# Optimization experiments

Hardware: AMD Instinct MI355X
Metric: run time of the kernel (lower is better)

Reference implementation:

```python
import jax, jax.numpy as jnp
import numpy as np

B, DIM, H, W, HEAD = 8, 512, 32, 32, 8
DH = DIM // HEAD
N = H * W


def setup_inputs() -> dict:
    key = jax.random.key(0)
    ks = jax.random.split(key, 9)
    s = 0.05  # keep conv-weight scale modest so softmax logits are sane
    return {
        "x": jax.random.normal(ks[0], (B, DIM, H, W), jnp.float32),
        "wq_w": jax.random.normal(ks[1], (DIM, DIM), jnp.float32) * s,
        "wq_b": jax.random.normal(ks[2], (DIM,), jnp.float32) * s,
        "wk_w": jax.random.normal(ks[3], (DIM, DIM), jnp.float32) * s,
        "wk_b": jax.random.normal(ks[4], (DIM,), jnp.float32) * s,
        "wv_w": jax.random.normal(ks[5], (DIM, DIM), jnp.float32) * s,
        "wv_b": jax.random.normal(ks[6], (DIM,), jnp.float32) * s,
        "r_h": jax.random.normal(ks[7], (1, HEAD, DH, 1, H), jnp.float32),
        "r_w": jax.random.normal(ks[8], (1, HEAD, DH, W, 1), jnp.float32),
    }


def reference(x, wq_w, wq_b, wk_w, wk_b, wv_w, wv_b, r_h, r_w):
    b, dim, h, w = x.shape
    head = r_h.shape[1]
    dh = dim // head
    n = h * w

    def conv1x1(inp, wgt, bias):
        # 1x1 conv == channel-mixing matmul
        return jnp.einsum('bchw,oc->bohw', inp, wgt) + bias[None, :, None, None]

    q = conv1x1(x, wq_w, wq_b).reshape(b, head, dh, n).transpose(0, 1, 3, 2)  # [b,h,n,d]
    k = conv1x1(x, wk_w, wk_b).reshape(b, head, dh, n)                        # [b,h,d,n]
    v = conv1x1(x, wv_w, wv_b).reshape(b, head, dh, n)                        # [b,h,d,n]

    # relative position term: (1,head,dh,1,H)+(1,head,dh,W,1) -> (1,head,dh,W*H)
    r = (r_h + r_w).reshape(head, dh, n)

    content_position = jnp.einsum('bhnd,hdm->bhnm', q, r)
    content_content = jnp.einsum('bhnd,bhdm->bhnm', q, k)
    # faithful odd reduction: softmax over the whole flattened (head*n*n) per batch row
    energy = (content_content + content_position).reshape(b, -1)
    attention = jax.nn.softmax(energy, axis=-1).reshape(b, head, n, n)

    feature = jnp.einsum('bhdn,bhnm->bhdm', v, attention).reshape(b, dim, h, w)
    # AvgPool2d(kernel=2, stride=2)
    out = feature.reshape(b, dim, h // 2, 2, w // 2, 2).mean(axis=(3, 5))
    return out
```

## Files before the change

### kernel.cpp

```cpp
#include <hip/hip_runtime.h>
#include <hip/hip_bf16.h>
#include <math.h>

#define BB   8
#define DIMC 512
#define HEAD 8
#define DH   64
#define NN   1024
#define HW   32

typedef __attribute__((ext_vector_type(8))) __bf16 bf16x8;
typedef __attribute__((ext_vector_type(4))) float  f32x4;

#define MFMA16(a, b, c) __builtin_amdgcn_mfma_f32_16x16x32_bf16((a), (b), (c), 0, 0, 0)

__device__ __forceinline__ int SW(int row, int col) {
    return (row << 6) + (col ^ ((row & 7) << 3));
}

__device__ __forceinline__ unsigned short bfh(float v) {
    unsigned int u = __float_as_uint(v);
    return (unsigned short)((u + 0x7fffu + ((u >> 16) & 1u)) >> 16);
}
__device__ __forceinline__ float bf2f(unsigned short h) {
    return __uint_as_float(((unsigned int)h) << 16);
}

__global__ __launch_bounds__(256)
void prep_x(const float* __restrict__ x,
            unsigned short* __restrict__ XTh, unsigned short* __restrict__ XTl)
{
    const int tid = threadIdx.x;
    const int nt = blockIdx.x;
    const int ct = blockIdx.y;
    const int b  = blockIdx.z;
    const int c0 = ct << 6, n0 = nt << 6;

    __shared__ float XsT[64][68];

    #pragma unroll
    for (int p = 0; p < 4; ++p) {
        int idx = tid + (p << 8);
        int cr = idx >> 4;
        int nc4 = (idx & 15) << 2;
        float4 v = *(const float4*)&x[((size_t)b * DIMC + c0 + cr) * NN + n0 + nc4];
        XsT[nc4 + 0][cr] = v.x;
        XsT[nc4 + 1][cr] = v.y;
        XsT[nc4 + 2][cr] = v.z;
        XsT[nc4 + 3][cr] = v.w;
    }
    __syncthreads();
    #pragma unroll
    for (int p = 0; p < 4; ++p) {
        int idx = tid + (p << 8);
        int n = idx >> 4;
        int c4 = (idx & 15) << 2;
        float4 v = *(const float4*)&XsT[n][c4];
        float vv[4] = {v.x, v.y, v.z, v.w};
        union { unsigned short u[4]; uint2 w; } ph, pl;
        #pragma unroll
        for (int j = 0; j < 4; ++j) {
            unsigned short hh = bfh(vv[j]);
            ph.u[j] = hh;
            pl.u[j] = bfh(vv[j] - bf2f(hh));
        }
        size_t off = ((size_t)(b * NN + n0 + n)) * DIMC + c0 + c4;
        *(uint2*)&XTh[off] = ph.w;
        *(uint2*)&XTl[off] = pl.w;
    }
}

__global__ __launch_bounds__(256)
void prep_w(const float* __restrict__ wq, const float* __restrict__ wk,
            const float* __restrict__ wv,
            unsigned short* __restrict__ Wh, unsigned short* __restrict__ Wl)
{
    const int z = blockIdx.y;
    const float* src = (z == 0) ? wq : (z == 1) ? wk : wv;
    const size_t zb = (size_t)z * DIMC * DIMC;
    #pragma unroll
    for (int p = 0; p < 4; ++p) {
        size_t i = (size_t)blockIdx.x * 4096 + (p << 10) + (threadIdx.x << 2);
        float4 v = *(const float4*)&src[i];
        float vv[4] = {v.x, v.y, v.z, v.w};
        union { unsigned short u[4]; uint2 w; } ph, pl;
        #pragma unroll
        for (int j = 0; j < 4; ++j) {
            unsigned short hh = bfh(vv[j]);
            ph.u[j] = hh;
            pl.u[j] = bfh(vv[j] - bf2f(hh));
        }
        *(uint2*)&Wh[zb + i] = ph.w;
        *(uint2*)&Wl[zb + i] = pl.w;
    }
}

__global__ __launch_bounds__(256)
void qkv_gemm(const unsigned short* __restrict__ XTh, const unsigned short* __restrict__ XTl,
              const unsigned short* __restrict__ Wh, const unsigned short* __restrict__ Wl,
              const float* __restrict__ wq_b, const float* __restrict__ wk_b,
              const float* __restrict__ wv_b,
              const float* __restrict__ r_h, const float* __restrict__ r_w,
              unsigned short* __restrict__ Qh, unsigned short* __restrict__ Ql,
              unsigned short* __restrict__ Kh, unsigned short* __restrict__ Kl,
              unsigned short* __restrict__ Vh, unsigned short* __restrict__ Vl)
{
    const int tid = threadIdx.x;
    const int z = blockIdx.z, hd = blockIdx.y;
    const int gn = blockIdx.x << 7;
    const int b = gn >> 10, posb = gn & 1023;
    const int oB = hd << 6;
    const int lane = tid & 63, w = tid >> 6;

    __shared__ __align__(16) unsigned short sm[24576];
    unsigned short* Ah = sm;
    unsigned short* Al = sm + 4096;
    unsigned short* Bh = sm + 8192;
    unsigned short* Bl = sm + 16384;

    const float* bias = (z == 0) ? wq_b : (z == 1) ? wk_b : wv_b;
    const unsigned short* wsh = Wh + (size_t)z * DIMC * DIMC + (size_t)oB * DIMC;
    const unsigned short* wsl = Wl + (size_t)z * DIMC * DIMC + (size_t)oB * DIMC;
    const unsigned short* xth = XTh + ((size_t)(b * NN + posb)) * DIMC;
    const unsigned short* xtl = XTl + ((size_t)(b * NN + posb)) * DIMC;

    f32x4 acc[8];
    #pragma unroll
    for (int t = 0; t < 8; ++t) acc[t] = (f32x4){0.f, 0.f, 0.f, 0.f};

    for (int ks = 0; ks < 8; ++ks) {
        const int c0 = ks << 6;
        #pragma unroll
        for (int p = 0; p < 2; ++p) {
            int idx = (p << 8) + tid;
            int row = idx >> 3, col8 = (idx & 7) << 3;
            size_t g = (size_t)row * DIMC + c0 + col8;
            *(float4*)&Ah[SW(row, col8)] = *(const float4*)&wsh[g];
            *(float4*)&Al[SW(row, col8)] = *(const float4*)&wsl[g];
        }
        #pragma unroll
        for (int p = 0; p < 4; ++p) {
            int idx = (p << 8) + tid;
            int row = idx >> 3, col8 = (idx & 7) << 3;
            size_t g = (size_t)row * DIMC + c0 + col8;
            *(float4*)&Bh[SW(row, col8)] = *(const float4*)&xth[g];
            *(float4*)&Bl[SW(row, col8)] = *(const float4*)&xtl[g];
        }
        __syncthreads();

        const int ar = (w << 4) + (lane & 15);
        const int kc = (lane >> 4) << 3;
        bf16x8 ah[2], al[2];
        ah[0] = *(const bf16x8*)&Ah[SW(ar, kc)];
        ah[1] = *(const bf16x8*)&Ah[SW(ar, 32 + kc)];
        al[0] = *(const bf16x8*)&Al[SW(ar, kc)];
        al[1] = *(const bf16x8*)&Al[SW(ar, 32 + kc)];
        #pragma unroll
        for (int t = 0; t < 8; ++t) {
            int br = (t << 4) + (lane & 15);
            #pragma unroll
            for (int s = 0; s < 2; ++s) {
                bf16x8 xh = *(const bf16x8*)&Bh[SW(br, s * 32 + kc)];
                bf16x8 xl = *(const bf16x8*)&Bl[SW(br, s * 32 + kc)];
                acc[t] = MFMA16(ah[s], xh, acc[t]);
                acc[t] = MFMA16(ah[s], xl, acc[t]);
                acc[t] = MFMA16(al[s], xh, acc[t]);
            }
        }
        __syncthreads();
    }

    float* F = (float*)sm;
    #pragma unroll
    for (int t = 0; t < 8; ++t) {
        int n = (t << 4) + (lane & 15);
        #pragma unroll
        for (int r = 0; r < 4; ++r) {
            int o = (w << 4) + ((lane >> 4) << 2) + r;
            F[o * 132 + n] = acc[t][r];
        }
    }
    __syncthreads();

    const size_t bh = (size_t)(b * HEAD + hd);
    if (z != 2) {
        unsigned short* Dh = (z == 0) ? Qh : Kh;
        unsigned short* Dl = (z == 0) ? Ql : Kl;
        #pragma unroll
        for (int p = 0; p < 8; ++p) {
            int idx = (p << 8) + tid;
            int n = idx >> 4, d0 = (idx & 15) << 2;
            union { unsigned short u[4]; uint2 v; } ph, pl;
            #pragma unroll
            for (int i = 0; i < 4; ++i) {
                int d = d0 + i;
                float val = F[d * 132 + n] + bias[oB + d];
                if (z == 1) {
                    int m = posb + n;
                    val += r_h[(size_t)(oB + d) * HW + (m & 31)]
                         + r_w[(size_t)(oB + d) * HW + (m >> 5)];
                }
                unsigned short hh = bfh(val);
                ph.u[i] = hh;
                pl.u[i] = bfh(val - bf2f(hh));
            }
            size_t off = (((size_t)bh * NN + posb + n) << 6) + d0;
            *(uint2*)&Dh[off] = ph.v;
            *(uint2*)&Dl[off] = pl.v;
        }
    } else {
        #pragma unroll
        for (int p = 0; p < 8; ++p) {
            int idx = (p << 8) + tid;
            int d = idx >> 5, n0 = (idx & 31) << 2;
            float4 v = *(const float4*)&F[d * 132 + n0];
            float vv[4] = {v.x, v.y, v.z, v.w};
            float bia = bias[oB + d];
            union { unsigned short u[4]; uint2 w2; } ph, pl;
            #pragma unroll
            for (int j = 0; j < 4; ++j) {
                float val = vv[j] + bia;
                unsigned short hh = bfh(val);
                ph.u[j] = hh;
                pl.u[j] = bfh(val - bf2f(hh));
            }
            size_t off = (((size_t)bh << 6) + d) * NN + posb + n0;
            *(uint2*)&Vh[off] = ph.w2;
            *(uint2*)&Vl[off] = pl.w2;
        }
    }
}

__global__ __launch_bounds__(256)
void stats_kernel(const unsigned short* __restrict__ Qh, const unsigned short* __restrict__ Ql,
                  const unsigned short* __restrict__ Kh, const unsigned short* __restrict__ Kl,
                  float* __restrict__ pstats)
{
    const int tid = threadIdx.x;
    const int mt = blockIdx.x, hd = blockIdx.y, b = blockIdx.z;
    const int mBase = mt << 6;
    const int bh = b * HEAD + hd;
    const int lane = tid & 63;
    const int w = tid >> 6;

    __shared__ __align__(16) unsigned short sm[8192];
    unsigned short* Th = sm;
    unsigned short* Tl = sm + 4096;

    {
        const unsigned short* kh = Kh + (((size_t)bh * NN + mBase) << 6);
        const unsigned short* kl = Kl + (((size_t)bh * NN + mBase) << 6);
        #pragma unroll
        for (int p = 0; p < 2; ++p) {
            int idx = (p << 8) + tid;
            int row = idx >> 3, c8 = (idx & 7) << 3;
            *(float4*)&Th[SW(row, c8)] = *(const float4*)&kh[(row << 6) + c8];
            *(float4*)&Tl[SW(row, c8)] = *(const float4*)&kl[(row << 6) + c8];
        }
    }
    __syncthreads();
    bf16x8 kfh[4][2], kfl[4][2];
    {
        const int r0 = lane & 15, c0 = (lane >> 4) << 3;
        #pragma unroll
        for (int t = 0; t < 4; ++t)
            #pragma unroll
            for (int s = 0; s < 2; ++s) {
                kfh[t][s] = *(const bf16x8*)&Th[SW(t * 16 + r0, s * 32 + c0)];
                kfl[t][s] = *(const bf16x8*)&Tl[SW(t * 16 + r0, s * 32 + c0)];
            }
    }
    __syncthreads();

    const unsigned short* qh = Qh + ((size_t)bh * NN << 6);
    const unsigned short* ql = Ql + ((size_t)bh * NN << 6);

    float m_r = -1e30f, s_r = 0.f;

    for (int nt = 0; nt < 16; ++nt) {
        const int nB = nt << 6;
        #pragma unroll
        for (int p = 0; p < 2; ++p) {
            int idx = (p << 8) + tid;
            int row = idx >> 3, c8 = (idx & 7) << 3;
            *(float4*)&Th[SW(row, c8)] = *(const float4*)&qh[((size_t)(nB + row) << 6) + c8];
            *(float4*)&Tl[SW(row, c8)] = *(const float4*)&ql[((size_t)(nB + row) << 6) + c8];
        }
        __syncthreads();

        f32x4 sacc[4];
        #pragma unroll
        for (int t = 0; t < 4; ++t) sacc[t] = (f32x4){0.f, 0.f, 0.f, 0.f};

        #pragma unroll
        for (int s = 0; s < 2; ++s) {
            int ar = (w << 4) + (lane & 15);
            int ac = s * 32 + ((lane >> 4) << 3);
            bf16x8 ah = *(const bf16x8*)&Th[SW(ar, ac)];
            bf16x8 al = *(const bf16x8*)&Tl[SW(ar, ac)];
            #pragma unroll
            for (int t = 0; t < 4; ++t) {
                sacc[t] = MFMA16(ah, kfh[t][s], sacc[t]);
                sacc[t] = MFMA16(ah, kfl[t][s], sacc[t]);
                sacc[t] = MFMA16(al, kfh[t][s], sacc[t]);
            }
        }

        float tmax = -1e30f;
        #pragma unroll
        for (int t = 0; t < 4; ++t)
            #pragma unroll
            for (int r = 0; r < 4; ++r) tmax = fmaxf(tmax, sacc[t][r]);
        float nm = fmaxf(m_r, tmax);
        s_r *= __expf(m_r - nm);
        float tt = 0.f;
        #pragma unroll
        for (int t = 0; t < 4; ++t)
            #pragma unroll
            for (int r = 0; r < 4; ++r) tt += __expf(sacc[t][r] - nm);
        s_r += tt;
        m_r = nm;
        __syncthreads();
    }

    float* red = (float*)sm;
    red[tid] = m_r;
    red[256 + tid] = s_r;
    __syncthreads();
    for (int off = 128; off > 0; off >>= 1) {
        if (tid < off) {
            float m2 = red[tid + off], s2 = red[256 + tid + off];
            float M = fmaxf(red[tid], m2);
            red[256 + tid] = red[256 + tid] * __expf(red[tid] - M) + s2 * __expf(m2 - M);
            red[tid] = M;
        }
        __syncthreads();
    }
    if (tid == 0) {
        pstats[((b << 7) + (hd << 4) + mt) * 2 + 0] = red[0];
        pstats[((b << 7) + (hd << 4) + mt) * 2 + 1] = red[256];
    }
}

__global__ __launch_bounds__(128)
void combine_kernel(const float* __restrict__ pstats, float* __restrict__ gstats)
{
    const int b = blockIdx.x, tid = threadIdx.x;
    __shared__ float rm[128], rs[128];
    rm[tid] = pstats[((b << 7) + tid) * 2 + 0];
    rs[tid] = pstats[((b << 7) + tid) * 2 + 1];
    __syncthreads();
    for (int off = 64; off > 0; off >>= 1) {
        if (tid < off) {
            float m2 = rm[tid + off], s2 = rs[tid + off];
            float M = fmaxf(rm[tid], m2);
            rs[tid] = rs[tid] * __expf(rm[tid] - M) + s2 * __expf(m2 - M);
            rm[tid] = M;
        }
        __syncthreads();
    }
    if (tid == 0) { gstats[b * 2] = rm[0]; gstats[b * 2 + 1] = rs[0]; }
}

__global__ __launch_bounds__(256)
void pv_kernel(const unsigned short* __restrict__ Qh, const unsigned short* __restrict__ Ql,
               const unsigned short* __restrict__ Kh, const unsigned short* __restrict__ Kl,
               const unsigned short* __restrict__ Vh, const unsigned short* __restrict__ Vl,
               const float* __restrict__ gstats, float* __restrict__ out)
{
    const int tid = threadIdx.x;
    const int mt = blockIdx.x, hd = blockIdx.y, b = blockIdx.z;
    const int mBase = mt << 6;
    const int bh = b * HEAD + hd;
    const int lane = tid & 63;
    const int w = tid >> 6;

    __shared__ __align__(16) unsigned short sm[24576];
    unsigned short* Qsh = sm;
    unsigned short* Qsl = sm + 4096;
    unsigned short* Vsh = sm + 8192;
    unsigned short* Vsl = sm + 12288;
    unsigned short* Ash = sm + 16384;
    unsigned short* Asl = sm + 20480;

    {
        const unsigned short* kh = Kh + (((size_t)bh * NN + mBase) << 6);
        const unsigned short* kl = Kl + (((size_t)bh * NN + mBase) << 6);
        #pragma unroll
        for (int p = 0; p < 2; ++p) {
            int idx = (p << 8) + tid;
            int row = idx >> 3, c8 = (idx & 7) << 3;
            *(float4*)&Ash[SW(row, c8)] = *(const float4*)&kh[(row << 6) + c8];
            *(float4*)&Asl[SW(row, c8)] = *(const float4*)&kl[(row << 6) + c8];
        }
    }
    __syncthreads();
    bf16x8 kfh[4][2], kfl[4][2];
    {
        const int r0 = lane & 15, c0 = (lane >> 4) << 3;
        #pragma unroll
        for (int t = 0; t < 4; ++t)
            #pragma unroll
            for (int s = 0; s < 2; ++s) {
                kfh[t][s] = *(const bf16x8*)&Ash[SW(t * 16 + r0, s * 32 + c0)];
                kfl[t][s] = *(const bf16x8*)&Asl[SW(t * 16 + r0, s * 32 + c0)];
            }
    }
    __syncthreads();

    const unsigned short* qh = Qh + ((size_t)bh * NN << 6);
    const unsigned short* ql = Ql + ((size_t)bh * NN << 6);
    const unsigned short* vh = Vh + (((size_t)bh << 6) * NN);
    const unsigned short* vl = Vl + (((size_t)bh << 6) * NN);

    const float gmax = gstats[b * 2];
    const float ginv = 1.f / gstats[b * 2 + 1];

    f32x4 facc[4];
    #pragma unroll
    for (int t = 0; t < 4; ++t) facc[t] = (f32x4){0.f, 0.f, 0.f, 0.f};

    for (int nt = 0; nt < 16; ++nt) {
        const int nB = nt << 6;
        #pragma unroll
        for (int p = 0; p < 2; ++p) {
            int idx = (p << 8) + tid;
            int row = idx >> 3, c8 = (idx & 7) << 3;
            *(float4*)&Qsh[SW(row, c8)] = *(const float4*)&qh[((size_t)(nB + row) << 6) + c8];
            *(float4*)&Qsl[SW(row, c8)] = *(const float4*)&ql[((size_t)(nB + row) << 6) + c8];
            *(float4*)&Vsh[SW(row, c8)] = *(const float4*)&vh[(size_t)row * NN + nB + c8];
            *(float4*)&Vsl[SW(row, c8)] = *(const float4*)&vl[(size_t)row * NN + nB + c8];
        }
        __syncthreads();

        f32x4 sacc[4];
        #pragma unroll
        for (int t = 0; t < 4; ++t) sacc[t] = (f32x4){0.f, 0.f, 0.f, 0.f};
        #pragma unroll
        for (int s = 0; s < 2; ++s) {
            int ar = (w << 4) + (lane & 15);
            int ac = s * 32 + ((lane >> 4) << 3);
            bf16x8 ah = *(const bf16x8*)&Qsh[SW(ar, ac)];
            bf16x8 al = *(const bf16x8*)&Qsl[SW(ar, ac)];
            #pragma unroll
            for (int t = 0; t < 4; ++t) {
                sacc[t] = MFMA16(ah, kfh[t][s], sacc[t]);
                sacc[t] = MFMA16(ah, kfl[t][s], sacc[t]);
                sacc[t] = MFMA16(al, kfh[t][s], sacc[t]);
            }
        }

        {
            const int c0 = lane & 15;
            const int g4 = (lane >> 4) << 2;
            #pragma unroll
            for (int t = 0; t < 4; ++t) {
                union { unsigned short u[4]; uint2 v; } ph, pl;
                #pragma unroll
                for (int r = 0; r < 4; ++r) {
                    float wv = __expf(sacc[t][r] - gmax) * ginv;
                    unsigned short hh = bfh(wv);
                    ph.u[r] = hh;
                    pl.u[r] = bfh(wv - bf2f(hh));
                }
                int mrow = t * 16 + c0;
                int ncol = (w << 4) + g4;
                *(uint2*)&Ash[SW(mrow, ncol)] = ph.v;
                *(uint2*)&Asl[SW(mrow, ncol)] = pl.v;
            }
        }
        __syncthreads();

        #pragma unroll
        for (int s = 0; s < 2; ++s) {
            int ar = (w << 4) + (lane & 15);
            int ac = s * 32 + ((lane >> 4) << 3);
            bf16x8 pah = *(const bf16x8*)&Ash[SW(ar, ac)];
            bf16x8 pal = *(const bf16x8*)&Asl[SW(ar, ac)];
            #pragma unroll
            for (int t = 0; t < 4; ++t) {
                int vr = t * 16 + (lane & 15);
                bf16x8 vvh = *(const bf16x8*)&Vsh[SW(vr, ac)];
                bf16x8 vvl = *(const bf16x8*)&Vsl[SW(vr, ac)];
                facc[t] = MFMA16(pah, vvh, facc[t]);
                facc[t] = MFMA16(pah, vvl, facc[t]);
                facc[t] = MFMA16(pal, vvh, facc[t]);
            }
        }
        __syncthreads();
    }

    float* F = (float*)sm;
    #pragma unroll
    for (int t = 0; t < 4; ++t) {
        int d = t * 16 + (lane & 15);
        #pragma unroll
        for (int r = 0; r < 4; ++r) {
            int m = (w << 4) + ((lane >> 4) << 2) + r;
            F[(m << 6) + d] = facc[t][r];
        }
    }
    __syncthreads();
    #pragma unroll
    for (int q = 0; q < 4; ++q) {
        int idx = (tid << 2) + q;
        int d = idx >> 4, wo = idx & 15;
        float v = 0.25f * (F[((wo << 1) << 6) + d] + F[(((wo << 1) + 1) << 6) + d] +
                           F[((32 + (wo << 1)) << 6) + d] + F[((33 + (wo << 1)) << 6) + d]);
        out[(((size_t)(b * DIMC + (hd << 6) + d) << 4) + mt) * 16 + wo] = v;
    }
}

extern "C" void kernel_launch(void* const* d_in, const int* in_sizes, int n_in,
                              void* d_out, int out_size, void* d_ws, size_t ws_size,
                              hipStream_t stream)
{
    const float* x    = (const float*)d_in[0];
    const float* wq_w = (const float*)d_in[1];
    const float* wq_b = (const float*)d_in[2];
    const float* wk_w = (const float*)d_in[3];
    const float* wk_b = (const float*)d_in[4];
    const float* wv_w = (const float*)d_in[5];
    const float* wv_b = (const float*)d_in[6];
    const float* r_h  = (const float*)d_in[7];
    const float* r_w  = (const float*)d_in[8];
    float* out = (float*)d_out;

    const size_t PRN = (size_t)BB * HEAD * NN * DH;
    const size_t WSZ = (size_t)3 * DIMC * DIMC;
    unsigned short* Qh  = (unsigned short*)d_ws;
    unsigned short* Ql  = Qh + PRN;
    unsigned short* Kh  = Ql + PRN;
    unsigned short* Kl  = Kh + PRN;
    unsigned short* Vh  = Kl + PRN;
    unsigned short* Vl  = Vh + PRN;
    unsigned short* XTh = Vl + PRN;
    unsigned short* XTl = XTh + PRN;
    unsigned short* Wh  = XTl + PRN;
    unsigned short* Wl  = Wh + WSZ;
    float* pstats = (float*)(Wl + WSZ);
    float* gstats = pstats + BB * 128 * 2;

    prep_x<<<dim3(16, 8, 8), 256, 0, stream>>>(x, XTh, XTl);
    prep_w<<<dim3(64, 3), 256, 0, stream>>>(wq_w, wk_w, wv_w, Wh, Wl);
    qkv_gemm<<<dim3(64, 8, 3), 256, 0, stream>>>(XTh, XTl, Wh, Wl,
                                                 wq_b, wk_b, wv_b, r_h, r_w,
                                                 Qh, Ql, Kh, Kl, Vh, Vl);
    stats_kernel<<<dim3(16, 8, 8), 256, 0, stream>>>(Qh, Ql, Kh, Kl, pstats);
    combine_kernel<<<dim3(8), 128, 0, stream>>>(pstats, gstats);
    pv_kernel<<<dim3(16, 8, 8), 256, 0, stream>>>(Qh, Ql, Kh, Kl, Vh, Vl, gstats, out);
}
```

Before: 298.6 us.

## Keep attention probabilities in registers and load Q fragments directly from global

The stats and PV kernels now load K and Q MFMA fragments straight from global memory into registers instead of staging them through swizzled LDS, which drops shared-memory traffic and several barriers. In the PV kernel the softmax probabilities stay in registers and feed a 16x16x16 bf16 MFMA as the B operand, so the probability tile is no longer written to and reread from LDS. Each wave now accumulates a partial output over its own slice of the n dimension, and the four waves' partials are summed through padded LDS at the end. In exchange the PV kernel holds four times as many accumulator registers and issues more, smaller MFMAs, and occupancy hints are added to both kernels.

```diff
diff --git a/kernel.cpp b/kernel.cpp
--- a/kernel.cpp
+++ b/kernel.cpp
@@ -11,8 +11,19 @@
 
 typedef __attribute__((ext_vector_type(8))) __bf16 bf16x8;
 typedef __attribute__((ext_vector_type(4))) float  f32x4;
+typedef __attribute__((ext_vector_type(4))) short  short4v;
 
 #define MFMA16(a, b, c) __builtin_amdgcn_mfma_f32_16x16x32_bf16((a), (b), (c), 0, 0, 0)
+
+__device__ __forceinline__ f32x4 mfma_pv(short4v a, short4v b, f32x4 c) {
+#if __has_builtin(__builtin_amdgcn_mfma_f32_16x16x16bf16_1k)
+    return __builtin_amdgcn_mfma_f32_16x16x16bf16_1k(a, b, c, 0, 0, 0);
+#else
+    asm volatile("v_mfma_f32_16x16x16_bf16 %0, %1, %2, %0"
+                 : "+v"(c) : "v"(a), "v"(b));
+    return c;
+#endif
+}
 
 __device__ __forceinline__ int SW(int row, int col) {
     return (row << 6) + (col ^ ((row & 7) << 3));
@@ -231,79 +242,58 @@
     }
 }
 
-__global__ __launch_bounds__(256)
+__global__ __launch_bounds__(256, 4)
 void stats_kernel(const unsigned short* __restrict__ Qh, const unsigned short* __restrict__ Ql,
                   const unsigned short* __restrict__ Kh, const unsigned short* __restrict__ Kl,
                   float* __restrict__ pstats)
 {
     const int tid = threadIdx.x;
     const int mt = blockIdx.x, hd = blockIdx.y, b = blockIdx.z;
-    const int mBase = mt << 6;
     const int bh = b * HEAD + hd;
-    const int lane = tid & 63;
-    const int w = tid >> 6;
-
-    __shared__ __align__(16) unsigned short sm[8192];
-    unsigned short* Th = sm;
-    unsigned short* Tl = sm + 4096;
-
-    {
-        const unsigned short* kh = Kh + (((size_t)bh * NN + mBase) << 6);
-        const unsigned short* kl = Kl + (((size_t)bh * NN + mBase) << 6);
-        #pragma unroll
-        for (int p = 0; p < 2; ++p) {
-            int idx = (p << 8) + tid;
-            int row = idx >> 3, c8 = (idx & 7) << 3;
-            *(float4*)&Th[SW(row, c8)] = *(const float4*)&kh[(row << 6) + c8];
-            *(float4*)&Tl[SW(row, c8)] = *(const float4*)&kl[(row << 6) + c8];
-        }
-    }
-    __syncthreads();
+    const int lane = tid & 63, w = tid >> 6;
+    const int r0 = lane & 15, c0 = (lane >> 4) << 3;
+
+    __shared__ float red[512];
+
+    const unsigned short* kh = Kh + (((size_t)bh * NN + (mt << 6)) << 6);
+    const unsigned short* kl = Kl + (((size_t)bh * NN + (mt << 6)) << 6);
     bf16x8 kfh[4][2], kfl[4][2];
-    {
-        const int r0 = lane & 15, c0 = (lane >> 4) << 3;
-        #pragma unroll
-        for (int t = 0; t < 4; ++t)
-            #pragma unroll
-            for (int s = 0; s < 2; ++s) {
-                kfh[t][s] = *(const bf16x8*)&Th[SW(t * 16 + r0, s * 32 + c0)];
-                kfl[t][s] = *(const bf16x8*)&Tl[SW(t * 16 + r0, s * 32 + c0)];
-            }
-    }
-    __syncthreads();
-
-    const unsigned short* qh = Qh + ((size_t)bh * NN << 6);
-    const unsigned short* ql = Ql + ((size_t)bh * NN << 6);
+    #pragma unroll
+    for (int t = 0; t < 4; ++t)
+        #pragma unroll
+        for (int s = 0; s < 2; ++s) {
+            int off = (((t << 4) + r0) << 6) + (s << 5) + c0;
+            kfh[t][s] = *(const bf16x8*)&kh[off];
+            kfl[t][s] = *(const bf16x8*)&kl[off];
+        }
+
+    const unsigned short* qh = Qh + (((size_t)bh * NN) << 6);
+    const unsigned short* ql = Ql + (((size_t)bh * NN) << 6);
 
     float m_r = -1e30f, s_r = 0.f;
 
     for (int nt = 0; nt < 16; ++nt) {
-        const int nB = nt << 6;
-        #pragma unroll
-        for (int p = 0; p < 2; ++p) {
-            int idx = (p << 8) + tid;
-            int row = idx >> 3, c8 = (idx & 7) << 3;
-            *(float4*)&Th[SW(row, c8)] = *(const float4*)&qh[((size_t)(nB + row) << 6) + c8];
-            *(float4*)&Tl[SW(row, c8)] = *(const float4*)&ql[((size_t)(nB + row) << 6) + c8];
-        }
-        __syncthreads();
+        const int qrow = (nt << 6) + (w << 4) + r0;
+        const size_t qb = ((size_t)qrow << 6) + c0;
+        bf16x8 ah0 = *(const bf16x8*)&qh[qb];
+        bf16x8 ah1 = *(const bf16x8*)&qh[qb + 32];
+        bf16x8 al0 = *(const bf16x8*)&ql[qb];
+        bf16x8 al1 = *(const bf16x8*)&ql[qb + 32];
 
         f32x4 sacc[4];
         #pragma unroll
         for (int t = 0; t < 4; ++t) sacc[t] = (f32x4){0.f, 0.f, 0.f, 0.f};
-
-        #pragma unroll
-        for (int s = 0; s < 2; ++s) {
-            int ar = (w << 4) + (lane & 15);
-            int ac = s * 32 + ((lane >> 4) << 3);
-            bf16x8 ah = *(const bf16x8*)&Th[SW(ar, ac)];
-            bf16x8 al = *(const bf16x8*)&Tl[SW(ar, ac)];
-            #pragma unroll
-            for (int t = 0; t < 4; ++t) {
-                sacc[t] = MFMA16(ah, kfh[t][s], sacc[t]);
-                sacc[t] = MFMA16(ah, kfl[t][s], sacc[t]);
-                sacc[t] = MFMA16(al, kfh[t][s], sacc[t]);
-            }
+        #pragma unroll
+        for (int t = 0; t < 4; ++t) {
+            sacc[t] = MFMA16(ah0, kfh[t][0], sacc[t]);
+            sacc[t] = MFMA16(ah0, kfl[t][0], sacc[t]);
+            sacc[t] = MFMA16(al0, kfh[t][0], sacc[t]);
+        }
+        #pragma unroll
+        for (int t = 0; t < 4; ++t) {
+            sacc[t] = MFMA16(ah1, kfh[t][1], sacc[t]);
+            sacc[t] = MFMA16(ah1, kfl[t][1], sacc[t]);
+            sacc[t] = MFMA16(al1, kfh[t][1], sacc[t]);
         }
 
         float tmax = -1e30f;
@@ -320,10 +310,8 @@
             for (int r = 0; r < 4; ++r) tt += __expf(sacc[t][r] - nm);
         s_r += tt;
         m_r = nm;
-        __syncthreads();
-    }
-
-    float* red = (float*)sm;
+    }
+
     red[tid] = m_r;
     red[256 + tid] = s_r;
     __syncthreads();
@@ -362,7 +350,7 @@
     if (tid == 0) { gstats[b * 2] = rm[0]; gstats[b * 2 + 1] = rs[0]; }
 }
 
-__global__ __launch_bounds__(256)
+__global__ __launch_bounds__(256, 2)
 void pv_kernel(const unsigned short* __restrict__ Qh, const unsigned short* __restrict__ Ql,
                const unsigned short* __restrict__ Kh, const unsigned short* __restrict__ Kl,
                const unsigned short* __restrict__ Vh, const unsigned short* __restrict__ Vl,
@@ -370,143 +358,138 @@
 {
     const int tid = threadIdx.x;
     const int mt = blockIdx.x, hd = blockIdx.y, b = blockIdx.z;
-    const int mBase = mt << 6;
     const int bh = b * HEAD + hd;
-    const int lane = tid & 63;
-    const int w = tid >> 6;
-
-    __shared__ __align__(16) unsigned short sm[24576];
-    unsigned short* Qsh = sm;
-    unsigned short* Qsl = sm + 4096;
-    unsigned short* Vsh = sm + 8192;
-    unsigned short* Vsl = sm + 12288;
-    unsigned short* Ash = sm + 16384;
-    unsigned short* Asl = sm + 20480;
-
-    {
-        const unsigned short* kh = Kh + (((size_t)bh * NN + mBase) << 6);
-        const unsigned short* kl = Kl + (((size_t)bh * NN + mBase) << 6);
+    const int lane = tid & 63, w = tid >> 6;
+    const int r0 = lane & 15, c0 = (lane >> 4) << 3;
+
+    __shared__ __align__(16) unsigned char smraw[2 * 64 * 65 * 4];
+    unsigned short* Vsh = (unsigned short*)smraw;
+    unsigned short* Vsl = Vsh + 4096;
+    float* F0 = (float*)smraw;
+    float* F1 = F0 + 64 * 65;
+
+    const unsigned short* kh = Kh + (((size_t)bh * NN + (mt << 6)) << 6);
+    const unsigned short* kl = Kl + (((size_t)bh * NN + (mt << 6)) << 6);
+    bf16x8 kfh[4][2], kfl[4][2];
+    #pragma unroll
+    for (int t = 0; t < 4; ++t)
+        #pragma unroll
+        for (int s = 0; s < 2; ++s) {
+            int off = (((t << 4) + r0) << 6) + (s << 5) + c0;
+            kfh[t][s] = *(const bf16x8*)&kh[off];
+            kfl[t][s] = *(const bf16x8*)&kl[off];
+        }
+
+    const unsigned short* qh = Qh + (((size_t)bh * NN) << 6);
+    const unsigned short* ql = Ql + (((size_t)bh * NN) << 6);
+    const unsigned short* vh = Vh + (((size_t)bh << 6) * NN);
+    const unsigned short* vl = Vl + (((size_t)bh << 6) * NN);
+
+    const float gmax = gstats[b * 2];
+    const float ginv = 1.f / gstats[b * 2 + 1];
+
+    f32x4 facc[4][4];
+    #pragma unroll
+    for (int u = 0; u < 4; ++u)
+        #pragma unroll
+        for (int t = 0; t < 4; ++t) facc[u][t] = (f32x4){0.f, 0.f, 0.f, 0.f};
+
+    for (int nt = 0; nt < 16; ++nt) {
+        const int nB = nt << 6;
         #pragma unroll
         for (int p = 0; p < 2; ++p) {
             int idx = (p << 8) + tid;
             int row = idx >> 3, c8 = (idx & 7) << 3;
-            *(float4*)&Ash[SW(row, c8)] = *(const float4*)&kh[(row << 6) + c8];
-            *(float4*)&Asl[SW(row, c8)] = *(const float4*)&kl[(row << 6) + c8];
-        }
-    }
-    __syncthreads();
-    bf16x8 kfh[4][2], kfl[4][2];
-    {
-        const int r0 = lane & 15, c0 = (lane >> 4) << 3;
-        #pragma unroll
-        for (int t = 0; t < 4; ++t)
-            #pragma unroll
-            for (int s = 0; s < 2; ++s) {
-                kfh[t][s] = *(const bf16x8*)&Ash[SW(t * 16 + r0, s * 32 + c0)];
-                kfl[t][s] = *(const bf16x8*)&Asl[SW(t * 16 + r0, s * 32 + c0)];
-            }
-    }
-    __syncthreads();
-
-    const unsigned short* qh = Qh + ((size_t)bh * NN << 6);
-    const unsigned short* ql = Ql + ((size_t)bh * NN << 6);
-    const unsigned short* vh = Vh + (((size_t)bh << 6) * NN);
-    const unsigned short* vl = Vl + (((size_t)bh << 6) * NN);
-
-    const float gmax = gstats[b * 2];
-    const float ginv = 1.f / gstats[b * 2 + 1];
-
-    f32x4 facc[4];
-    #pragma unroll
-    for (int t = 0; t < 4; ++t) facc[t] = (f32x4){0.f, 0.f, 0.f, 0.f};
-
-    for (int nt = 0; nt < 16; ++nt) {
-        const int nB = nt << 6;
-        #pragma unroll
-        for (int p = 0; p < 2; ++p) {
-            int idx = (p << 8) + tid;
-            int row = idx >> 3, c8 = (idx & 7) << 3;
-            *(float4*)&Qsh[SW(row, c8)] = *(const float4*)&qh[((size_t)(nB + row) << 6) + c8];
-            *(float4*)&Qsl[SW(row, c8)] = *(const float4*)&ql[((size_t)(nB + row) << 6) + c8];
             *(float4*)&Vsh[SW(row, c8)] = *(const float4*)&vh[(size_t)row * NN + nB + c8];
             *(float4*)&Vsl[SW(row, c8)] = *(const float4*)&vl[(size_t)row * NN + nB + c8];
         }
+        const int qrow = nB + (w << 4) + r0;
+        const size_t qb = ((size_t)qrow << 6) + c0;
+        bf16x8 ah0 = *(const bf16x8*)&qh[qb];
+        bf16x8 ah1 = *(const bf16x8*)&qh[qb + 32];
+        bf16x8 al0 = *(const bf16x8*)&ql[qb];
+        bf16x8 al1 = *(const bf16x8*)&ql[qb + 32];
         __syncthreads();
 
         f32x4 sacc[4];
         #pragma unroll
         for (int t = 0; t < 4; ++t) sacc[t] = (f32x4){0.f, 0.f, 0.f, 0.f};
         #pragma unroll
-        for (int s = 0; s < 2; ++s) {
-            int ar = (w << 4) + (lane & 15);
-            int ac = s * 32 + ((lane >> 4) << 3);
-            bf16x8 ah = *(const bf16x8*)&Qsh[SW(ar, ac)];
-            bf16x8 al = *(const bf16x8*)&Qsl[SW(ar, ac)];
+        for (int t = 0; t < 4; ++t) {
+            sacc[t] = MFMA16(ah0, kfh[t][0], sacc[t]);
+            sacc[t] = MFMA16(ah0, kfl[t][0], sacc[t]);
+            sacc[t] = MFMA16(al0, kfh[t][0], sacc[t]);
+        }
+        #pragma unroll
+        for (int t = 0; t < 4; ++t) {
+            sacc[t] = MFMA16(ah1, kfh[t][1], sacc[t]);
+            sacc[t] = MFMA16(ah1, kfl[t][1], sacc[t]);
+            sacc[t] = MFMA16(al1, kfh[t][1], sacc[t]);
+        }
+
+        short4v pah[4], pal[4];
+        #pragma unroll
+        for (int t = 0; t < 4; ++t) {
+            union { unsigned short u[4]; short4v v; } Ph, Pl;
+            #pragma unroll
+            for (int r = 0; r < 4; ++r) {
+                float a = __expf(sacc[t][r] - gmax) * ginv;
+                unsigned short hh = bfh(a);
+                Ph.u[r] = hh;
+                Pl.u[r] = bfh(a - bf2f(hh));
+            }
+            pah[t] = Ph.v;
+            pal[t] = Pl.v;
+        }
+
+        const int vcol = (w << 4) + ((lane >> 4) << 2);
+        #pragma unroll
+        for (int u = 0; u < 4; ++u) {
+            int vrow = (u << 4) + r0;
+            short4v vah = *(const short4v*)&Vsh[SW(vrow, vcol)];
+            short4v vbl = *(const short4v*)&Vsl[SW(vrow, vcol)];
             #pragma unroll
             for (int t = 0; t < 4; ++t) {
-                sacc[t] = MFMA16(ah, kfh[t][s], sacc[t]);
-                sacc[t] = MFMA16(ah, kfl[t][s], sacc[t]);
-                sacc[t] = MFMA16(al, kfh[t][s], sacc[t]);
+                facc[u][t] = mfma_pv(vah, pah[t], facc[u][t]);
+                facc[u][t] = mfma_pv(vbl, pah[t], facc[u][t]);
+                facc[u][t] = mfma_pv(vah, pal[t], facc[u][t]);
             }
         }
-
-        {
-            const int c0 = lane & 15;
-            const int g4 = (lane >> 4) << 2;
-            #pragma unroll
-            for (int t = 0; t < 4; ++t) {
-                union { unsigned short u[4]; uint2 v; } ph, pl;
+        __syncthreads();
+    }
+
+    const int fr = (lane >> 4) << 2;
+    if (w < 2) {
+        float* Fw = (w == 0) ? F0 : F1;
+        #pragma unroll
+        for (int u = 0; u < 4; ++u)
+            #pragma unroll
+            for (int t = 0; t < 4; ++t)
                 #pragma unroll
-                for (int r = 0; r < 4; ++r) {
-                    float wv = __expf(sacc[t][r] - gmax) * ginv;
-                    unsigned short hh = bfh(wv);
-                    ph.u[r] = hh;
-                    pl.u[r] = bfh(wv - bf2f(hh));
-                }
-                int mrow = t * 16 + c0;
-                int ncol = (w << 4) + g4;
-                *(uint2*)&Ash[SW(mrow, ncol)] = ph.v;
-                *(uint2*)&Asl[SW(mrow, ncol)] = pl.v;
-            }
-        }
-        __syncthreads();
-
-        #pragma unroll
-        for (int s = 0; s < 2; ++s) {
-            int ar = (w << 4) + (lane & 15);
-            int ac = s * 32 + ((lane >> 4) << 3);
-            bf16x8 pah = *(const bf16x8*)&Ash[SW(ar, ac)];
-            bf16x8 pal = *(const bf16x8*)&Asl[SW(ar, ac)];
-            #pragma unroll
-            for (int t = 0; t < 4; ++t) {
-                int vr = t * 16 + (lane & 15);
-                bf16x8 vvh = *(const bf16x8*)&Vsh[SW(vr, ac)];
-                bf16x8 vvl = *(const bf16x8*)&Vsl[SW(vr, ac)];
-                facc[t] = MFMA16(pah, vvh, facc[t]);
-                facc[t] = MFMA16(pah, vvl, facc[t]);
-                facc[t] = MFMA16(pal, vvh, facc[t]);
-            }
-        }
-        __syncthreads();
-    }
-
-    float* F = (float*)sm;
-    #pragma unroll
-    for (int t = 0; t < 4; ++t) {
-        int d = t * 16 + (lane & 15);
-        #pragma unroll
-        for (int r = 0; r < 4; ++r) {
-            int m = (w << 4) + ((lane >> 4) << 2) + r;
-            F[(m << 6) + d] = facc[t][r];
-        }
+                for (int r = 0; r < 4; ++r)
+                    Fw[((u << 4) + fr + r) * 65 + (t << 4) + r0] = facc[u][t][r];
+    }
+    __syncthreads();
+    if (w >= 2) {
+        float* Fw = (w == 2) ? F0 : F1;
+        #pragma unroll
+        for (int u = 0; u < 4; ++u)
+            #pragma unroll
+            for (int t = 0; t < 4; ++t)
+                #pragma unroll
+                for (int r = 0; r < 4; ++r)
+                    Fw[((u << 4) + fr + r) * 65 + (t << 4) + r0] += facc[u][t][r];
     }
     __syncthreads();
     #pragma unroll
     for (int q = 0; q < 4; ++q) {
         int idx = (tid << 2) + q;
         int d = idx >> 4, wo = idx & 15;
-        float v = 0.25f * (F[((wo << 1) << 6) + d] + F[(((wo << 1) + 1) << 6) + d] +
-                           F[((32 + (wo << 1)) << 6) + d] + F[((33 + (wo << 1)) << 6) + d]);
+        int m0 = wo << 1;
+        float v = 0.25f * ((F0[d * 65 + m0]      + F1[d * 65 + m0]) +
+                           (F0[d * 65 + m0 + 1]  + F1[d * 65 + m0 + 1]) +
+                           (F0[d * 65 + 32 + m0] + F1[d * 65 + 32 + m0]) +
+                           (F0[d * 65 + 33 + m0] + F1[d * 65 + 33 + m0]));
         out[(((size_t)(b * DIMC + (hd << 6) + d) << 4) + mt) * 16 + wo] = v;
     }
 }
```

After: 256.9 us. 14.0% less time.
